# Optimization experiments

Hardware: AMD Instinct MI355X
Metric: run time of the kernel (lower is better)

Reference implementation:

```python
import jax, jax.numpy as jnp
import numpy as np

B, C, N = 4, 256, 512
CQ = C // 4
SIGMA = 15.0
PICK = 0  # args.picked_point_num
FACTOR = 180.0 / (np.pi * SIGMA)
BN_EPS = 1e-5


def _angle_embed(angles, W, b):
    """SinusoidalPositionalEmbedding (interleaved sin/cos, detached) + Linear proj."""
    d = W.shape[0]
    div_term = jnp.exp(jnp.arange(0, d, 2, dtype=jnp.float32) * (-np.log(10000.0) / d))
    omegas = (angles * FACTOR)[..., None] * div_term  # (..., d/2)
    # torch cat([sin, cos], dim=2) on (-1, d/2, 1) then view -> interleaved [s0,c0,s1,c1,...]
    emb = jnp.stack([jnp.sin(omegas), jnp.cos(omegas)], axis=-1).reshape(*angles.shape, d)
    emb = jax.lax.stop_gradient(emb)  # .detach() in torch
    return emb @ W.T + b


def setup_inputs() -> dict:
    key = jax.random.key(0)
    ks = jax.random.split(key, 16)
    s = 0.05
    return {
        "x": jax.random.normal(ks[0], (B, C, N), jnp.float32),
        "pca": jax.random.normal(ks[1], (B, C, N), jnp.float32),
        "angle_lrf": jax.random.uniform(ks[2], (B, N, N), jnp.float32, 0.0, np.pi),
        "angle_pca": jax.random.uniform(ks[3], (B, N), jnp.float32, 0.0, np.pi),
        "Wkp": jax.random.normal(ks[4], (CQ, C), jnp.float32) * s,
        "Wk": jax.random.normal(ks[5], (CQ, C), jnp.float32) * s,
        "Wv": jax.random.normal(ks[6], (C, C), jnp.float32) * s,
        "Wvp": jax.random.normal(ks[7], (C, C), jnp.float32) * s,
        "emb1_W": jax.random.normal(ks[8], (CQ, CQ), jnp.float32) * s,
        "emb1_b": jnp.zeros((CQ,), jnp.float32),
        "emb2_W": jax.random.normal(ks[9], (CQ, CQ), jnp.float32) * s,
        "emb2_b": jnp.zeros((CQ,), jnp.float32),
        "lin_W": jax.random.normal(ks[10], (C, C), jnp.float32) * s,
        "lin_b": jnp.zeros((C,), jnp.float32),
        "bn_gamma": jnp.ones((C,), jnp.float32),
        "bn_beta": jnp.zeros((C,), jnp.float32),
    }


def reference(x, pca, angle_lrf, angle_pca, Wkp, Wk, Wv, Wvp,
              emb1_W, emb1_b, emb2_W, emb2_b, lin_W, lin_b, bn_gamma, bn_beta):
    # q uses the k_conv_pca weight (weight tying in __init__)
    x_q = jnp.einsum('oc,bcn->bno', Wkp, x)            # (B,N,CQ)
    k_lrf = jnp.einsum('oc,bcn->bon', Wk, x)           # (B,CQ,N)
    k_pca = jnp.einsum('oc,bcn->bon', Wkp, pca)        # (B,CQ,N)
    energy_lrf = jnp.einsum('bno,bom->bnm', x_q, k_lrf)
    energy_pca = jnp.einsum('bno,bom->bnm', x_q, k_pca)
    e1 = _angle_embed(angle_lrf, emb1_W, emb1_b)       # (B,N,N,CQ) relative-angle bias
    energy_lrf = energy_lrf + jnp.einsum('bnc,bnmc->bnm', x_q, e1)
    e2 = _angle_embed(angle_pca, emb2_W, emb2_b)       # (B,N,CQ)
    energy_pca = energy_pca + jnp.einsum('bnc,bmc->bnm', x_q, e2)
    energy = jax.nn.softmax(energy_lrf + energy_pca, axis=-1)
    # extra column renormalization
    energy = energy / (1e-12 + energy.sum(axis=1, keepdims=True))
    point_relation = energy[:, PICK:PICK + 1, :]       # (B,1,N)
    v_lrf = jnp.einsum('oc,bcn->bon', Wv, x)
    v_pca = jnp.einsum('oc,bcn->bon', Wvp, pca)
    x_lrf = jnp.einsum('bon,bnm->bom', v_lrf, energy)
    x_pca = jnp.einsum('bon,bnm->bom', v_pca, energy)
    x_r = 0.5 * x_lrf + 0.5 * x_pca
    z = jnp.einsum('oc,bcn->bon', lin_W, x - x_r) + lin_b[None, :, None]
    # BatchNorm1d (training-mode batch stats, biased var)
    mu = z.mean(axis=(0, 2), keepdims=True)
    var = z.var(axis=(0, 2), keepdims=True)
    y = bn_gamma[None, :, None] * (z - mu) * jax.lax.rsqrt(var + BN_EPS) + bn_beta[None, :, None]
    out = x + jax.nn.gelu(y, approximate=False)
    return out, point_relation
```

## Files before the change

kernel.cpp:

```cpp
#include <hip/hip_runtime.h>
#include <math.h>

#define FCT_REV 0.6079271018540267f
#define DIVK 0.28782313662425575f

using bf16x8 = __attribute__((ext_vector_type(8))) short;
using f32x4  = __attribute__((ext_vector_type(4))) float;

__device__ inline short f2bf(float f) {
    union { float f; unsigned u; } v; v.f = f;
    unsigned r = v.u + 0x7FFFu + ((v.u >> 16) & 1u);
    return (short)(r >> 16);
}
__device__ inline float bf2f(short s) {
    union { unsigned u; float f; } v;
    v.u = ((unsigned)(unsigned short)s) << 16;
    return v.f;
}
__device__ inline unsigned pk2(float lo, float hi) {
    return ((unsigned)(unsigned short)f2bf(hi) << 16) | (unsigned)(unsigned short)f2bf(lo);
}
__device__ inline float sinrev(float x) {
    float r; asm("v_sin_f32 %0, %1" : "=v"(r) : "v"(x)); return r;
}
__device__ inline float cosrev(float x) {
    float r; asm("v_cos_f32 %0, %1" : "=v"(r) : "v"(x)); return r;
}

__global__ __launch_bounds__(256) void k_prep(
    const float* __restrict__ Wkp, const float* __restrict__ Wk,
    const float* __restrict__ Wv, const float* __restrict__ Wvp,
    const float* __restrict__ linW, const float* __restrict__ e1W,
    const float* __restrict__ e2W,
    const float* __restrict__ x, const float* __restrict__ pca,
    short* __restrict__ Wcatb, short* __restrict__ InTb,
    float* __restrict__ e2Wt, float* __restrict__ stat, float* __restrict__ colsum)
{
    __shared__ float ts[64][65];
    const int bid = blockIdx.x;
    const int t = threadIdx.x;
    if (bid < 176) {
        if (bid == 0) {
            for (int i = t; i < 2048; i += 256) colsum[i] = 0.f;
            for (int i = t; i < 512; i += 256) stat[i] = 0.f;
        } else if (bid == 1) {
            for (int i = t; i < 4096; i += 256) {
                int k = i >> 6, o = i & 63;
                e2Wt[k*64 + o] = e2W[o*64 + k];
            }
        }
        #pragma unroll
        for (int rr = 0; rr < 4; ++rr) {
            const int r = bid*4 + rr;
            for (int k = t; k < 512; k += 256) {
                float v = 0.f;
                if (r < 64) { if (k < 256) v = Wkp[r*256 + k]; }
                else if (r < 128) { int o = r-64;  v = (k<256) ? Wk[o*256+k]  : Wkp[o*256 + k-256]; }
                else if (r < 384) { int o = r-128; v = (k<256) ? Wv[o*256+k]  : Wvp[o*256 + k-256]; }
                else if (r < 640) { int o = r-384; if (k<256) v = linW[o*256+k]; }
                else {
                    int o = r-640;
                    if (k < 256) {
                        float a = 0.f;
                        for (int j = 0; j < 64; ++j) a = fmaf(e1W[j*64 + o], Wkp[j*256 + k], a);
                        v = a;
                    }
                }
                Wcatb[(size_t)r*512 + k] = f2bf(v);
            }
        }
    } else {
        const int id = bid - 176;
        const int b  = id >> 6;
        const int kt = (id >> 3) & 7;
        const int nt = id & 7;
        const int k0 = kt*64, n0 = nt*64;
        const float* src = (k0 < 256) ? (x + ((size_t)b*256 + k0)*512)
                                      : (pca + ((size_t)b*256 + (k0-256))*512);
        #pragma unroll
        for (int i = 0; i < 16; ++i) {
            int idx = t + 256*i;
            int r = idx >> 6, c = idx & 63;
            ts[r][c] = src[(size_t)r*512 + n0 + c];
        }
        __syncthreads();
        short* dst = InTb + (size_t)b*512*512;
        #pragma unroll
        for (int i = 0; i < 16; ++i) {
            int idx = t + 256*i;
            int n = idx >> 6, k = idx & 63;
            dst[(size_t)(n0+n)*512 + k0 + k] = f2bf(ts[k][n]);
        }
    }
}

__global__ __launch_bounds__(256) void k_gemm1(
    const short* __restrict__ Wcatb, const short* __restrict__ InTb,
    short* __restrict__ xqb, float* __restrict__ KtTf, short* __restrict__ vsumb,
    float* __restrict__ linx, float* __restrict__ q1T)
{
    const int bid = blockIdx.x;
    const int b  = bid / 176;
    const int rt = (bid / 16) % 11;
    const int ct = bid % 16;
    const int r0 = rt*64, c0 = ct*32;
    const int w = threadIdx.x >> 6, lane = threadIdx.x & 63;
    const int lr = lane & 15, lg = lane >> 4;

    const short* ap  = Wcatb + (size_t)(r0 + w*16 + lr)*512 + 8*lg;
    const short* bp0 = InTb + (size_t)b*512*512 + (size_t)(c0 + lr)*512 + 8*lg;
    const short* bp1 = bp0 + 16*512;

    f32x4 acc0 = {0.f,0.f,0.f,0.f}, acc1 = {0.f,0.f,0.f,0.f};
    #pragma unroll 4
    for (int kk = 0; kk < 512; kk += 32) {
        bf16x8 a  = *(const bf16x8*)(ap  + kk);
        bf16x8 b0 = *(const bf16x8*)(bp0 + kk);
        bf16x8 b1 = *(const bf16x8*)(bp1 + kk);
        acc0 = __builtin_amdgcn_mfma_f32_16x16x32_bf16(a, b0, acc0, 0, 0, 0);
        acc1 = __builtin_amdgcn_mfma_f32_16x16x32_bf16(a, b1, acc1, 0, 0, 0);
    }
    const int rowb = r0 + w*16 + lg*4;
    const int col0 = c0 + lr;
    if (r0 == 0) {
        #pragma unroll
        for (int j = 0; j < 4; ++j) {
            xqb[((size_t)b*512 + col0)*64 + rowb + j]      = f2bf(acc0[j]);
            xqb[((size_t)b*512 + col0 + 16)*64 + rowb + j] = f2bf(acc1[j]);
        }
    } else if (r0 == 64) {
        float4 v0 = {acc0[0], acc0[1], acc0[2], acc0[3]};
        float4 v1 = {acc1[0], acc1[1], acc1[2], acc1[3]};
        *(float4*)&KtTf[((size_t)b*512 + col0)*64 + rowb - 64]      = v0;
        *(float4*)&KtTf[((size_t)b*512 + col0 + 16)*64 + rowb - 64] = v1;
    } else if (r0 < 384) {
        #pragma unroll
        for (int j = 0; j < 4; ++j) {
            vsumb[((size_t)b*256 + rowb-128 + j)*512 + col0]      = f2bf(acc0[j]);
            vsumb[((size_t)b*256 + rowb-128 + j)*512 + col0 + 16] = f2bf(acc1[j]);
        }
    } else if (r0 < 640) {
        #pragma unroll
        for (int j = 0; j < 4; ++j) {
            linx[((size_t)b*256 + rowb-384 + j)*512 + col0]      = acc0[j];
            linx[((size_t)b*256 + rowb-384 + j)*512 + col0 + 16] = acc1[j];
        }
    } else {
        #pragma unroll
        for (int j = 0; j < 4; ++j) {
            q1T[((size_t)b*512 + col0)*64 + rowb-640 + j]      = acc0[j];
            q1T[((size_t)b*512 + col0 + 16)*64 + rowb-640 + j] = acc1[j];
        }
    }
}

__global__ __launch_bounds__(256) void k_e2t2(
    const float* __restrict__ angle_pca, const float* __restrict__ e2Wt,
    const float* __restrict__ KtTf, short* __restrict__ KtT)
{
    const int b  = blockIdx.x >> 3;
    const int m0 = (blockIdx.x & 7) * 64;
    __shared__ float embs[64][65];
    const int t = threadIdx.x;
    {
        const int m = t >> 2, q = t & 3;
        const float arev = angle_pca[b*512 + m0 + m] * FCT_REV;
        #pragma unroll
        for (int j = q*8; j < q*8+8; ++j) {
            float arg = arev * __expf(-(float)j * DIVK);
            embs[m][2*j]   = sinrev(arg);
            embs[m][2*j+1] = cosrev(arg);
        }
    }
    __syncthreads();
    const int lane = t & 63;
    const int wv = __builtin_amdgcn_readfirstlane(t >> 6);
    const int m = lane;
    float acc[16];
    const float* kt = KtTf + ((size_t)b*512 + m0 + m)*64 + 16*wv;
    #pragma unroll
    for (int oi = 0; oi < 16; ++oi) acc[oi] = kt[oi];
    const float* wbase = e2Wt + 16*wv;
    #pragma unroll 4
    for (int k = 0; k < 64; ++k) {
        const float em = embs[m][k];
        const float* wr = wbase + (size_t)k*64;
        #pragma unroll
        for (int oi = 0; oi < 16; ++oi) acc[oi] = fmaf(wr[oi], em, acc[oi]);
    }
    short* dst = KtT + ((size_t)b*512 + m0 + m)*64 + 16*wv;
    #pragma unroll
    for (int oi = 0; oi < 16; oi += 2)
        *(unsigned*)(dst + oi) = pk2(acc[oi], acc[oi+1]);
}

__global__ __launch_bounds__(256) void k_qk(
    const short* __restrict__ xqb, const short* __restrict__ KtT,
    float* __restrict__ S)
{
    const int bid = blockIdx.x;
    const int b  = bid / 128;
    const int rt = (bid / 16) % 8;
    const int ct = bid % 16;
    const int r0 = rt*64, c0 = ct*32;
    const int w = threadIdx.x >> 6, lane = threadIdx.x & 63;
    const int lr = lane & 15, lg = lane >> 4;
    const short* ap  = xqb + ((size_t)b*512 + r0 + w*16 + lr)*64 + 8*lg;
    const short* bp0 = KtT + ((size_t)b*512 + c0 + lr)*64 + 8*lg;
    const short* bp1 = bp0 + 16*64;
    f32x4 acc0 = {0.f,0.f,0.f,0.f}, acc1 = {0.f,0.f,0.f,0.f};
    #pragma unroll
    for (int kk = 0; kk < 64; kk += 32) {
        bf16x8 a  = *(const bf16x8*)(ap  + kk);
        bf16x8 b0 = *(const bf16x8*)(bp0 + kk);
        bf16x8 b1 = *(const bf16x8*)(bp1 + kk);
        acc0 = __builtin_amdgcn_mfma_f32_16x16x32_bf16(a, b0, acc0, 0, 0, 0);
        acc1 = __builtin_amdgcn_mfma_f32_16x16x32_bf16(a, b1, acc1, 0, 0, 0);
    }
    const int rowb = r0 + w*16 + lg*4;
    const int col0 = c0 + lr;
    float* Sb = S + (size_t)b*512*512;
    #pragma unroll
    for (int j = 0; j < 4; ++j) {
        Sb[(size_t)(rowb+j)*512 + col0]      = acc0[j];
        Sb[(size_t)(rowb+j)*512 + col0 + 16] = acc1[j];
    }
}

__global__ __launch_bounds__(256, 2) void k_energy2(
    const float* __restrict__ S, const float* __restrict__ q1T,
    const float* __restrict__ angle_lrf, short* __restrict__ ETb,
    float* __restrict__ colsum)
{
    const int b  = blockIdx.x >> 7;
    const int n0 = (blockIdx.x & 127) * 4;
    __shared__ float qs[4][64];
    __shared__ float divs[32];
    __shared__ float4 xw[4];
    const int t = threadIdx.x;
    if (t < 64) {
        #pragma unroll
        for (int i = 0; i < 4; ++i) qs[i][t] = q1T[((size_t)b*512 + n0 + i)*64 + t];
    } else if (t < 96) {
        divs[t-64] = __expf(-(float)(t-64) * DIVK);
    }
    __syncthreads();
    float acc[4][2], av[4][2];
    #pragma unroll
    for (int i = 0; i < 4; ++i) {
        const float2 sv = *(const float2*)&S[((size_t)b*512 + n0 + i)*512 + 2*t];
        const float2 an = *(const float2*)&angle_lrf[((size_t)b*512 + n0 + i)*512 + 2*t];
        acc[i][0] = sv.x; acc[i][1] = sv.y;
        av[i][0] = an.x * FCT_REV; av[i][1] = an.y * FCT_REV;
    }
    #pragma unroll 2
    for (int j = 0; j < 32; ++j) {
        const float d = divs[j];
        #pragma unroll
        for (int i = 0; i < 4; ++i) {
            const float q0 = qs[i][2*j], q1 = qs[i][2*j+1];
            #pragma unroll
            for (int m = 0; m < 2; ++m) {
                const float arg = av[i][m] * d;
                acc[i][m] = fmaf(q0, sinrev(arg), fmaf(q1, cosrev(arg), acc[i][m]));
            }
        }
    }
    float v0 = fmaxf(acc[0][0], acc[0][1]), v1 = fmaxf(acc[1][0], acc[1][1]);
    float v2 = fmaxf(acc[2][0], acc[2][1]), v3 = fmaxf(acc[3][0], acc[3][1]);
    #pragma unroll
    for (int off = 1; off < 64; off <<= 1) {
        v0 = fmaxf(v0, __shfl_xor(v0, off));
        v1 = fmaxf(v1, __shfl_xor(v1, off));
        v2 = fmaxf(v2, __shfl_xor(v2, off));
        v3 = fmaxf(v3, __shfl_xor(v3, off));
    }
    const int wid = t >> 6, lane = t & 63;
    if (lane == 0) { float4 f = {v0,v1,v2,v3}; xw[wid] = f; }
    __syncthreads();
    {
        const float4 a0 = xw[0], a1 = xw[1], a2 = xw[2], a3 = xw[3];
        v0 = fmaxf(fmaxf(a0.x,a1.x), fmaxf(a2.x,a3.x));
        v1 = fmaxf(fmaxf(a0.y,a1.y), fmaxf(a2.y,a3.y));
        v2 = fmaxf(fmaxf(a0.z,a1.z), fmaxf(a2.z,a3.z));
        v3 = fmaxf(fmaxf(a0.w,a1.w), fmaxf(a2.w,a3.w));
    }
    float p[4][2];
    p[0][0] = __expf(acc[0][0]-v0); p[0][1] = __expf(acc[0][1]-v0);
    p[1][0] = __expf(acc[1][0]-v1); p[1][1] = __expf(acc[1][1]-v1);
    p[2][0] = __expf(acc[2][0]-v2); p[2][1] = __expf(acc[2][1]-v2);
    p[3][0] = __expf(acc[3][0]-v3); p[3][1] = __expf(acc[3][1]-v3);
    float s0 = p[0][0]+p[0][1], s1 = p[1][0]+p[1][1];
    float s2 = p[2][0]+p[2][1], s3 = p[3][0]+p[3][1];
    #pragma unroll
    for (int off = 1; off < 64; off <<= 1) {
        s0 += __shfl_xor(s0, off); s1 += __shfl_xor(s1, off);
        s2 += __shfl_xor(s2, off); s3 += __shfl_xor(s3, off);
    }
    __syncthreads();
    if (lane == 0) { float4 f = {s0,s1,s2,s3}; xw[wid] = f; }
    __syncthreads();
    {
        const float4 a0 = xw[0], a1 = xw[1], a2 = xw[2], a3 = xw[3];
        s0 = (a0.x+a1.x) + (a2.x+a3.x);
        s1 = (a0.y+a1.y) + (a2.y+a3.y);
        s2 = (a0.z+a1.z) + (a2.z+a3.z);
        s3 = (a0.w+a1.w) + (a2.w+a3.w);
    }
    const float i0 = 1.f/s0, i1 = 1.f/s1, i2 = 1.f/s2, i3 = 1.f/s3;
    short* Eb = ETb + (size_t)b*512*512;
    #pragma unroll
    for (int m = 0; m < 2; ++m) {
        const float e0 = p[0][m]*i0, e1 = p[1][m]*i1, e2 = p[2][m]*i2, e3 = p[3][m]*i3;
        uint2 u;
        u.x = pk2(e0, e1);
        u.y = pk2(e2, e3);
        *(uint2*)(Eb + (size_t)(2*t + m)*512 + n0) = u;
        atomicAdd(&colsum[b*512 + 2*t + m], (e0 + e1) + (e2 + e3));
    }
}

__global__ __launch_bounds__(256) void k_xr2(
    const short* __restrict__ vsumb, const short* __restrict__ ETb,
    const float* __restrict__ colsum, short* __restrict__ xrT,
    float* __restrict__ out)
{
    const int bid = blockIdx.x;
    const int b  = bid / 64;
    const int rt = (bid / 16) % 4;
    const int ct = bid % 16;
    const int r0 = rt*64, c0 = ct*32;
    const int w = threadIdx.x >> 6, lane = threadIdx.x & 63;
    const int lr = lane & 15, lg = lane >> 4;
    const short* ap  = vsumb + (size_t)b*256*512 + (size_t)(r0 + w*16 + lr)*512 + 8*lg;
    const short* bp0 = ETb + (size_t)b*512*512 + (size_t)(c0 + lr)*512 + 8*lg;
    const short* bp1 = bp0 + 16*512;
    f32x4 acc0 = {0.f,0.f,0.f,0.f}, acc1 = {0.f,0.f,0.f,0.f};
    #pragma unroll 4
    for (int kk = 0; kk < 512; kk += 32) {
        bf16x8 a  = *(const bf16x8*)(ap  + kk);
        bf16x8 b0 = *(const bf16x8*)(bp0 + kk);
        bf16x8 b1 = *(const bf16x8*)(bp1 + kk);
        acc0 = __builtin_amdgcn_mfma_f32_16x16x32_bf16(a, b0, acc0, 0, 0, 0);
        acc1 = __builtin_amdgcn_mfma_f32_16x16x32_bf16(a, b1, acc1, 0, 0, 0);
    }
    const int rowb = r0 + w*16 + lg*4;
    const int m0 = c0 + lr, m1 = m0 + 16;
    const float rc0 = 1.f / (1e-12f + colsum[b*512 + m0]);
    const float rc1 = 1.f / (1e-12f + colsum[b*512 + m1]);
    const float s0 = 0.5f * rc0, s1 = 0.5f * rc1;
    short* xb = xrT + (size_t)b*512*256;
    uint2 u;
    u.x = pk2(acc0[0]*s0, acc0[1]*s0);
    u.y = pk2(acc0[2]*s0, acc0[3]*s0);
    *(uint2*)(xb + (size_t)m0*256 + rowb) = u;
    u.x = pk2(acc1[0]*s1, acc1[1]*s1);
    u.y = pk2(acc1[2]*s1, acc1[3]*s1);
    *(uint2*)(xb + (size_t)m1*256 + rowb) = u;
    if (w == 0 && lg == 0) {
        out[(size_t)4*256*512 + b*512 + m0] = bf2f(ETb[((size_t)b*512 + m0)*512]) * rc0;
        out[(size_t)4*256*512 + b*512 + m1] = bf2f(ETb[((size_t)b*512 + m1)*512]) * rc1;
    }
}

__global__ __launch_bounds__(256) void k_z2st(
    const short* __restrict__ Wcatb, const short* __restrict__ xrT,
    const float* __restrict__ linx, const float* __restrict__ lin_b,
    float* __restrict__ z, float* __restrict__ stat)
{
    const int bid = blockIdx.x;
    const int b  = bid / 64;
    const int rt = (bid / 16) % 4;
    const int ct = bid % 16;
    const int r0 = rt*64, c0 = ct*32;
    const int w = threadIdx.x >> 6, lane = threadIdx.x & 63;
    const int lr = lane & 15, lg = lane >> 4;
    const short* ap  = Wcatb + (size_t)(384 + r0 + w*16 + lr)*512 + 8*lg;
    const short* bp0 = xrT + (size_t)b*512*256 + (size_t)(c0 + lr)*256 + 8*lg;
    const short* bp1 = bp0 + 16*256;
    f32x4 acc0 = {0.f,0.f,0.f,0.f}, acc1 = {0.f,0.f,0.f,0.f};
    #pragma unroll
    for (int kk = 0; kk < 256; kk += 32) {
        bf16x8 a  = *(const bf16x8*)(ap  + kk);
        bf16x8 b0 = *(const bf16x8*)(bp0 + kk);
        bf16x8 b1 = *(const bf16x8*)(bp1 + kk);
        acc0 = __builtin_amdgcn_mfma_f32_16x16x32_bf16(a, b0, acc0, 0, 0, 0);
        acc1 = __builtin_amdgcn_mfma_f32_16x16x32_bf16(a, b1, acc1, 0, 0, 0);
    }
    const int rowb = r0 + w*16 + lg*4;
    const int col0 = c0 + lr;
    const float* Lb = linx + (size_t)b*256*512;
    float* zb = z + (size_t)b*256*512;
    #pragma unroll
    for (int j = 0; j < 4; ++j) {
        const float lb = lin_b[rowb+j];
        const float z0 = Lb[(size_t)(rowb+j)*512 + col0]      - acc0[j] + lb;
        const float z1 = Lb[(size_t)(rowb+j)*512 + col0 + 16] - acc1[j] + lb;
        zb[(size_t)(rowb+j)*512 + col0]      = z0;
        zb[(size_t)(rowb+j)*512 + col0 + 16] = z1;
        float s  = z0 + z1;
        float s2 = z0*z0 + z1*z1;
        #pragma unroll
        for (int off = 1; off < 16; off <<= 1) {
            s  += __shfl_xor(s,  off);
            s2 += __shfl_xor(s2, off);
        }
        if (lr == 0) {
            atomicAdd(&stat[rowb+j], s);
            atomicAdd(&stat[256 + rowb+j], s2);
        }
    }
}

__global__ __launch_bounds__(256) void k_final(
    const float* __restrict__ x, const float* __restrict__ z,
    const float* __restrict__ stat, const float* __restrict__ gamma,
    const float* __restrict__ beta, float* __restrict__ out)
{
    const int gid = blockIdx.x*256 + threadIdx.x;
    const int base = gid * 4;
    const int c = (base >> 9) & 255;
    const float mu  = stat[c] * (1.f/2048.f);
    const float var = stat[256 + c] * (1.f/2048.f) - mu*mu;
    const float gsc = gamma[c] * rsqrtf(var + 1e-5f);
    const float bt  = beta[c];
    const float4 zv = *(const float4*)&z[base];
    const float4 xv = *(const float4*)&x[base];
    float4 ov;
    {
        float y = (zv.x - mu)*gsc + bt;
        ov.x = xv.x + 0.5f*y*(1.f + erff(y*0.70710678118654752f));
        y = (zv.y - mu)*gsc + bt;
        ov.y = xv.y + 0.5f*y*(1.f + erff(y*0.70710678118654752f));
        y = (zv.z - mu)*gsc + bt;
        ov.z = xv.z + 0.5f*y*(1.f + erff(y*0.70710678118654752f));
        y = (zv.w - mu)*gsc + bt;
        ov.w = xv.w + 0.5f*y*(1.f + erff(y*0.70710678118654752f));
    }
    *(float4*)&out[base] = ov;
}

extern "C" void kernel_launch(void* const* d_in, const int* in_sizes, int n_in,
                              void* d_out, int out_size, void* d_ws, size_t ws_size,
                              hipStream_t stream)
{
    const float* x         = (const float*)d_in[0];
    const float* pca       = (const float*)d_in[1];
    const float* angle_lrf = (const float*)d_in[2];
    const float* angle_pca = (const float*)d_in[3];
    const float* Wkp       = (const float*)d_in[4];
    const float* Wk        = (const float*)d_in[5];
    const float* Wv        = (const float*)d_in[6];
    const float* Wvp       = (const float*)d_in[7];
    const float* e1W       = (const float*)d_in[8];
    const float* e2W       = (const float*)d_in[10];
    const float* linW      = (const float*)d_in[12];
    const float* linb      = (const float*)d_in[13];
    const float* gamma     = (const float*)d_in[14];
    const float* beta      = (const float*)d_in[15];

    char* w = (char*)d_ws;
    short* Wcatb  = (short*)(w + 0);
    short* InTb   = (short*)(w + 720896);
    short* vsumb  = (short*)(w + 2818048);
    short* KtT    = (short*)(w + 3866624);
    short* ETb    = (short*)(w + 4128768);
    short* xrT    = (short*)(w + 6225920);
    float* stat   = (float*)(w + 7274496);
    float* colsum = (float*)(w + 7276544);
    float* S      = (float*)(w + 7284736);
    float* e2Wt   = (float*)(w + 7284736);
    float* z      = (float*)(w + 7284736);
    float* KtTf   = (float*)(w + 11479040);
    short* xqb    = (short*)(w + 12003328);
    float* q1T    = (float*)(w + 12265472);
    float* linx   = (float*)(w + 12789760);
    float* out    = (float*)d_out;

    k_prep   <<<432, 256, 0, stream>>>(Wkp, Wk, Wv, Wvp, linW, e1W, e2W, x, pca,
                                       Wcatb, InTb, e2Wt, stat, colsum);
    k_gemm1  <<<704, 256, 0, stream>>>(Wcatb, InTb, xqb, KtTf, vsumb, linx, q1T);
    k_e2t2   <<<32,  256, 0, stream>>>(angle_pca, e2Wt, KtTf, KtT);
    k_qk     <<<512, 256, 0, stream>>>(xqb, KtT, S);
    k_energy2<<<512, 256, 0, stream>>>(S, q1T, angle_lrf, ETb, colsum);
    k_xr2    <<<256, 256, 0, stream>>>(vsumb, ETb, colsum, xrT, out);
    k_z2st   <<<256, 256, 0, stream>>>(Wcatb, xrT, linx, linb, z, stat);
    k_final  <<<512, 256, 0, stream>>>(x, z, stat, gamma, beta, out);
}
```

Baseline: 89.16 us.

## Fuse angle_pca embedding projection into gemm1 epilogue, drop k_e2t2 kernel

Folds the sinusoidal angle_pca embedding and its 64x64 projection into the K-tile blocks of the first GEMM, so those blocks write bf16 KtT directly. This removes one kernel launch and the fp32 KtTf round trip through global memory. In exchange, every gemm1 block allocates about 24KB of shared memory and the K blocks do extra scalar FMA work, which may reduce occupancy. It also drops the min-blocks hint from k_energy2's launch bounds.

```diff
diff --git a/kernel.cpp b/kernel.cpp
--- a/kernel.cpp
+++ b/kernel.cpp
@@ -96,9 +96,12 @@
 
 __global__ __launch_bounds__(256) void k_gemm1(
     const short* __restrict__ Wcatb, const short* __restrict__ InTb,
-    short* __restrict__ xqb, float* __restrict__ KtTf, short* __restrict__ vsumb,
+    const float* __restrict__ angle_pca, const float* __restrict__ e2Wt,
+    short* __restrict__ xqb, short* __restrict__ KtT, short* __restrict__ vsumb,
     float* __restrict__ linx, float* __restrict__ q1T)
 {
+    __shared__ float embs[32][65];
+    __shared__ float e2ws[64][64];
     const int bid = blockIdx.x;
     const int b  = bid / 176;
     const int rt = (bid / 16) % 11;
@@ -106,6 +109,23 @@
     const int r0 = rt*64, c0 = ct*32;
     const int w = threadIdx.x >> 6, lane = threadIdx.x & 63;
     const int lr = lane & 15, lg = lane >> 4;
+    const int t = threadIdx.x;
+
+    if (r0 == 64) {
+        const int mloc = t >> 3, q = t & 7;
+        const float arev = angle_pca[b*512 + c0 + mloc] * FCT_REV;
+        #pragma unroll
+        for (int j = q*4; j < q*4+4; ++j) {
+            const float arg = arev * __expf(-(float)j * DIVK);
+            embs[mloc][2*j]   = sinrev(arg);
+            embs[mloc][2*j+1] = cosrev(arg);
+        }
+        #pragma unroll
+        for (int i = 0; i < 16; ++i) {
+            const int idx = t + 256*i;
+            e2ws[idx >> 6][idx & 63] = e2Wt[idx];
+        }
+    }
 
     const short* ap  = Wcatb + (size_t)(r0 + w*16 + lr)*512 + 8*lg;
     const short* bp0 = InTb + (size_t)b*512*512 + (size_t)(c0 + lr)*512 + 8*lg;
@@ -129,10 +149,29 @@
             xqb[((size_t)b*512 + col0 + 16)*64 + rowb + j] = f2bf(acc1[j]);
         }
     } else if (r0 == 64) {
-        float4 v0 = {acc0[0], acc0[1], acc0[2], acc0[3]};
-        float4 v1 = {acc1[0], acc1[1], acc1[2], acc1[3]};
-        *(float4*)&KtTf[((size_t)b*512 + col0)*64 + rowb - 64]      = v0;
-        *(float4*)&KtTf[((size_t)b*512 + col0 + 16)*64 + rowb - 64] = v1;
+        __syncthreads();
+        const int o0 = w*16 + lg*4;
+        float e[8];
+        #pragma unroll
+        for (int i = 0; i < 8; ++i) e[i] = 0.f;
+        #pragma unroll 8
+        for (int k = 0; k < 64; ++k) {
+            const float em0 = embs[lr][k];
+            const float em1 = embs[lr + 16][k];
+            #pragma unroll
+            for (int j = 0; j < 4; ++j) {
+                const float wv = e2ws[k][o0 + j];
+                e[j]     = fmaf(wv, em0, e[j]);
+                e[4 + j] = fmaf(wv, em1, e[4 + j]);
+            }
+        }
+        uint2 u0, u1;
+        u0.x = pk2(acc0[0] + e[0], acc0[1] + e[1]);
+        u0.y = pk2(acc0[2] + e[2], acc0[3] + e[3]);
+        u1.x = pk2(acc1[0] + e[4], acc1[1] + e[5]);
+        u1.y = pk2(acc1[2] + e[6], acc1[3] + e[7]);
+        *(uint2*)(KtT + ((size_t)b*512 + col0)*64 + o0)      = u0;
+        *(uint2*)(KtT + ((size_t)b*512 + col0 + 16)*64 + o0) = u1;
     } else if (r0 < 384) {
         #pragma unroll
         for (int j = 0; j < 4; ++j) {
@@ -152,46 +191,6 @@
             q1T[((size_t)b*512 + col0 + 16)*64 + rowb-640 + j] = acc1[j];
         }
     }
-}
-
-__global__ __launch_bounds__(256) void k_e2t2(
-    const float* __restrict__ angle_pca, const float* __restrict__ e2Wt,
-    const float* __restrict__ KtTf, short* __restrict__ KtT)
-{
-    const int b  = blockIdx.x >> 3;
-    const int m0 = (blockIdx.x & 7) * 64;
-    __shared__ float embs[64][65];
-    const int t = threadIdx.x;
-    {
-        const int m = t >> 2, q = t & 3;
-        const float arev = angle_pca[b*512 + m0 + m] * FCT_REV;
-        #pragma unroll
-        for (int j = q*8; j < q*8+8; ++j) {
-            float arg = arev * __expf(-(float)j * DIVK);
-            embs[m][2*j]   = sinrev(arg);
-            embs[m][2*j+1] = cosrev(arg);
-        }
-    }
-    __syncthreads();
-    const int lane = t & 63;
-    const int wv = __builtin_amdgcn_readfirstlane(t >> 6);
-    const int m = lane;
-    float acc[16];
-    const float* kt = KtTf + ((size_t)b*512 + m0 + m)*64 + 16*wv;
-    #pragma unroll
-    for (int oi = 0; oi < 16; ++oi) acc[oi] = kt[oi];
-    const float* wbase = e2Wt + 16*wv;
-    #pragma unroll 4
-    for (int k = 0; k < 64; ++k) {
-        const float em = embs[m][k];
-        const float* wr = wbase + (size_t)k*64;
-        #pragma unroll
-        for (int oi = 0; oi < 16; ++oi) acc[oi] = fmaf(wr[oi], em, acc[oi]);
-    }
-    short* dst = KtT + ((size_t)b*512 + m0 + m)*64 + 16*wv;
-    #pragma unroll
-    for (int oi = 0; oi < 16; oi += 2)
-        *(unsigned*)(dst + oi) = pk2(acc[oi], acc[oi+1]);
 }
 
 __global__ __launch_bounds__(256) void k_qk(
@@ -227,7 +226,7 @@
     }
 }
 
-__global__ __launch_bounds__(256, 2) void k_energy2(
+__global__ __launch_bounds__(256) void k_energy2(
     const float* __restrict__ S, const float* __restrict__ q1T,
     const float* __restrict__ angle_lrf, short* __restrict__ ETb,
     float* __restrict__ colsum)
@@ -471,7 +470,6 @@
     float* S      = (float*)(w + 7284736);
     float* e2Wt   = (float*)(w + 7284736);
     float* z      = (float*)(w + 7284736);
-    float* KtTf   = (float*)(w + 11479040);
     short* xqb    = (short*)(w + 12003328);
     float* q1T    = (float*)(w + 12265472);
     float* linx   = (float*)(w + 12789760);
@@ -479,8 +477,8 @@
 
     k_prep   <<<432, 256, 0, stream>>>(Wkp, Wk, Wv, Wvp, linW, e1W, e2W, x, pca,
                                        Wcatb, InTb, e2Wt, stat, colsum);
-    k_gemm1  <<<704, 256, 0, stream>>>(Wcatb, InTb, xqb, KtTf, vsumb, linx, q1T);
-    k_e2t2   <<<32,  256, 0, stream>>>(angle_pca, e2Wt, KtTf, KtT);
+    k_gemm1  <<<704, 256, 0, stream>>>(Wcatb, InTb, angle_pca, e2Wt,
+                                       xqb, KtT, vsumb, linx, q1T);
     k_qk     <<<512, 256, 0, stream>>>(xqb, KtT, S);
     k_energy2<<<512, 256, 0, stream>>>(S, q1T, angle_lrf, ETb, colsum);
     k_xr2    <<<256, 256, 0, stream>>>(vsumb, ETb, colsum, xrT, out);
```

Result: faster. 81.53 us (-8.6%).
